# Kernel optimization log

Measured on AMD Instinct MI355X. Metric: run time of the kernel, lower is better.

## Reference

```python
import jax, jax.numpy as jnp
import numpy as np

B, T, IN, H, OUT = 1024, 512, 19, 128, 7


def setup_inputs() -> dict:
    key = jax.random.key(0)
    ks = jax.random.split(key, 12)
    k = 1.0 / np.sqrt(H)  # torch default init bound for LSTMCell/Linear
    u = lambda kk, shape: jax.random.uniform(kk, shape, jnp.float32, -k, k)
    return {
        "x": jax.random.normal(ks[0], (B, T, IN), jnp.float32),
        "W_ih1": u(ks[1], (4 * H, IN)),
        "W_hh1": u(ks[2], (4 * H, H)),
        "b_ih1": u(ks[3], (4 * H,)),
        "b_hh1": u(ks[4], (4 * H,)),
        "W_ih2": u(ks[5], (4 * H, H)),
        "W_hh2": u(ks[6], (4 * H, H)),
        "b_ih2": u(ks[7], (4 * H,)),
        "b_hh2": u(ks[8], (4 * H,)),
        "W_lin": u(ks[9], (OUT, H)),
        "b_lin": u(ks[10], (OUT,)),
    }


def _lstm_cell(x_t, h, c, W_ih, W_hh, b_ih, b_hh):
    # gates in torch order: i, f, g, o
    gates = x_t @ W_ih.T + b_ih + h @ W_hh.T + b_hh  # [B, 4H]
    i, f, g, o = jnp.split(gates, 4, axis=-1)
    c_new = jax.nn.sigmoid(f) * c + jax.nn.sigmoid(i) * jnp.tanh(g)
    h_new = jax.nn.sigmoid(o) * jnp.tanh(c_new)
    return h_new, c_new


def reference(x, W_ih1, W_hh1, b_ih1, b_hh1, W_ih2, W_hh2, b_ih2, b_hh2, W_lin, b_lin):
    n = x.shape[0]
    z = jnp.zeros((n, H), jnp.float32)

    def step(carry, x_t):
        h1, c1, h2, c2 = carry
        h1, c1 = _lstm_cell(x_t, h1, c1, W_ih1, W_hh1, b_ih1, b_hh1)
        h2, c2 = _lstm_cell(h1, h2, c2, W_ih2, W_hh2, b_ih2, b_hh2)
        y = h2 @ W_lin.T + b_lin  # [B, OUT]
        return (h1, c1, h2, c2), y

    xs = jnp.swapaxes(x, 0, 1)  # [T, B, IN]
    _, ys = jax.lax.scan(step, (z, z, z, z), xs)  # ys: [T, B, OUT]
    # torch.cat(outputs, 1) -> [B, T*OUT]
    return jnp.swapaxes(ys, 0, 1).reshape(n, -1)
```

## Files before the change

kernel.cpp:

```cpp
#include <hip/hip_runtime.h>


typedef _Float16 half8 __attribute__((ext_vector_type(8)));
typedef float f32x4 __attribute__((ext_vector_type(4)));

#define MFMA16(a, b, c) __builtin_amdgcn_mfma_f32_16x16x32_f16((a), (b), (c), 0, 0, 0)
#define BARRIER() asm volatile("s_waitcnt lgkmcnt(0)\ns_barrier" ::: "memory")
#define D_AHEAD 4
#define NSLOT 5

__device__ __forceinline__ void pin(half8& v) { asm volatile("" : "+v"(v)); }

__device__ __forceinline__ void glds16(const _Float16* g, _Float16* l) {
  __builtin_amdgcn_global_load_lds(
      (const __attribute__((address_space(1))) void*)g,
      (__attribute__((address_space(3))) void*)l, 16, 0, 0);
}

__device__ __forceinline__ float sigf(float x) {
  return __builtin_amdgcn_rcpf(1.f + __expf(-x));
}
__device__ __forceinline__ float tanhf_(float x) {
  return 1.f - 2.f * __builtin_amdgcn_rcpf(1.f + __expf(2.f * x));
}
__device__ __forceinline__ float sel4(const f32x4 a, const int lg) {
  const float v01 = (lg & 1) ? a[1] : a[0];
  const float v23 = (lg & 1) ? a[3] : a[2];
  return (lg & 2) ? v23 : v01;
}

__global__ __launch_bounds__(512) void lstm_layer1_kernel(
    const float* __restrict__ x,
    const float* __restrict__ Wih,
    const float* __restrict__ Whh,
    const float* __restrict__ bih, const float* __restrict__ bhh,
    _Float16* __restrict__ h1g)
{
  __shared__ _Float16 xls[512][12][8];
  __shared__ _Float16 hbuf[2][64][8];
  const int tid = threadIdx.x, bid = blockIdx.x;
  const int wv = tid >> 6, lane = tid & 63;
  const int lg = lane >> 4, lc = lane & 15;
  const int col = wv * 16 + lc;
  const int off0 = lg * 32 + (lc & 3) * 8;
  const int woff = ((wv * 2 + (lc >> 3)) * 4 + lg) * 8 + (lc & 7);

  half8 wih_f[4], whh_f[4][4];
  float bias[4];
#pragma unroll
  for (int g = 0; g < 4; ++g) {
    const int n = g * 128 + col;
    bias[g] = bih[n] + bhh[n];
    half8 f;
#pragma unroll
    for (int j = 0; j < 8; ++j) {
      const int k = lg * 8 + j;
      f[j] = (_Float16)((k < 19) ? Wih[n * 19 + k] : 0.f);
    }
    wih_f[g] = f;
#pragma unroll
    for (int kk = 0; kk < 4; ++kk) {
      const float* p = Whh + n * 128 + kk * 32 + lg * 8;
      half8 f2;
#pragma unroll
      for (int j = 0; j < 8; ++j) f2[j] = (_Float16)p[j];
      whh_f[g][kk] = f2;
    }
  }

  for (int i2 = tid; i2 < 512 * 96; i2 += 512) {
    const int t = i2 / 96, r = i2 - t * 96;
    const int cc = r >> 5, rr = (r >> 3) & 3, j = r & 7;
    const int k = cc * 8 + j;
    float v = 0.f;
    if (k < 19) v = x[((size_t)(bid * 4 + rr) * 512 + t) * 19 + k];
    xls[t][cc * 4 + rr][j] = (_Float16)v;
  }
  for (int i = tid; i < 1024; i += 512) ((_Float16*)hbuf)[i] = (_Float16)0.f;
  __syncthreads();

  float c = 0.f;
  _Float16* h1p = h1g + (size_t)(bid * 4 + lg) * 128 + col;
  const _Float16* xb = &xls[0][0][0] + off0;
  _Float16* hb0p = &hbuf[0][0][0];
  const f32x4 fz = {0.f, 0.f, 0.f, 0.f};
  const bool xv = (lg < 3);

#define L1_STEP(T, RD, WR)                                                    \
  {                                                                           \
    const _Float16* rd = (RD) + off0;                                         \
    const half8 hb0 = *(const half8*)(rd);                                    \
    const half8 hb1 = *(const half8*)(rd + 128);                              \
    const half8 hb2 = *(const half8*)(rd + 256);                              \
    const half8 hb3 = *(const half8*)(rd + 384);                              \
    half8 ax = {};                                                            \
    if (xv) ax = *(const half8*)(xb + (T) * 96);                              \
    f32x4 a0 = MFMA16(ax, wih_f[0], fz);                                      \
    f32x4 a1 = MFMA16(ax, wih_f[1], fz);                                      \
    f32x4 a2 = MFMA16(ax, wih_f[2], fz);                                      \
    f32x4 a3 = MFMA16(ax, wih_f[3], fz);                                      \
    a0 = MFMA16(hb0, whh_f[0][0], a0); a1 = MFMA16(hb0, whh_f[1][0], a1);     \
    a2 = MFMA16(hb0, whh_f[2][0], a2); a3 = MFMA16(hb0, whh_f[3][0], a3);     \
    a0 = MFMA16(hb1, whh_f[0][1], a0); a1 = MFMA16(hb1, whh_f[1][1], a1);     \
    a2 = MFMA16(hb1, whh_f[2][1], a2); a3 = MFMA16(hb1, whh_f[3][1], a3);     \
    a0 = MFMA16(hb2, whh_f[0][2], a0); a1 = MFMA16(hb2, whh_f[1][2], a1);     \
    a2 = MFMA16(hb2, whh_f[2][2], a2); a3 = MFMA16(hb2, whh_f[3][2], a3);     \
    a0 = MFMA16(hb3, whh_f[0][3], a0); a1 = MFMA16(hb3, whh_f[1][3], a1);     \
    a2 = MFMA16(hb3, whh_f[2][3], a2); a3 = MFMA16(hb3, whh_f[3][3], a3);     \
    const float gi = sel4(a0, lg) + bias[0];                                  \
    const float gf = sel4(a1, lg) + bias[1];                                  \
    const float gg = sel4(a2, lg) + bias[2];                                  \
    const float go = sel4(a3, lg) + bias[3];                                  \
    const float I = sigf(gi), F = sigf(gf), G = tanhf_(gg), O = sigf(go);     \
    c = F * c + I * G;                                                        \
    const float h = O * tanhf_(c);                                            \
    const _Float16 h16 = (_Float16)h;                                         \
    (WR)[woff] = h16;                                                         \
    h1p[(size_t)(T) * 131072] = h16;                                          \
    BARRIER();                                                                \
  }

#pragma unroll 1
  for (int t = 0; t < 512; t += 2) {
    L1_STEP(t, hb0p + 512, hb0p);
    L1_STEP(t + 1, hb0p, hb0p + 512);
  }
#undef L1_STEP
}

__global__ __launch_bounds__(1024) void lstm_layer2_pc(
    const _Float16* __restrict__ h1g,
    const float* __restrict__ Wih,
    const float* __restrict__ Whh,
    const float* __restrict__ bih, const float* __restrict__ bhh,
    const float* __restrict__ Wlin,
    const float* __restrict__ blin,
    float* __restrict__ out)
{
  __shared__ float ring2[NSLOT][128 * 20];
  __shared__ _Float16 h1s[4][512];
  __shared__ _Float16 h2b[2][512];
  __shared__ _Float16 wlls[16][136];
  const int tid = threadIdx.x, bid = blockIdx.x;
  const int wv = tid >> 6, lane = tid & 63;
  const int lg = lane >> 4, lc = lane & 15;
  const bool isCons = (wv < 8);
  const int cw = isCons ? wv : (wv - 8);
  const int col = cw * 16 + lc;
  const int off0 = lg * 32 + (lc & 3) * 8;
  const int woff = ((col >> 3) * 4 + lg) * 8 + (col & 7);
  const int roff = col * 20 + lg * 4;

  for (int i = tid; i < 16 * 128; i += 1024)
    wlls[i >> 7][i & 127] = (_Float16)((i < 7 * 128) ? Wlin[i] : 0.f);
  for (int i = tid; i < 1024; i += 1024) ((_Float16*)h2b)[i] = (_Float16)0.f;

  const int gchunk = (lane & 48) | ((lane & 15) ^ ((lane >> 3) & 6));
  const _Float16* h1base = h1g + (size_t)bid * 512 + gchunk * 8;
  if (wv == 8) {
    glds16(h1base, &h1s[0][0]);
    glds16(h1base + 131072, &h1s[1][0]);
    glds16(h1base + 262144, &h1s[2][0]);
    asm volatile("s_waitcnt vmcnt(2)" ::: "memory");
  }

  if (isCons) {
    half8 wh_f[4][4];
#pragma unroll
    for (int g = 0; g < 4; ++g) {
      const int n = g * 128 + col;
#pragma unroll
      for (int kk = 0; kk < 4; ++kk) {
        const float* p = Whh + n * 128 + kk * 32 + lg * 8;
        half8 f;
#pragma unroll
        for (int j = 0; j < 8; ++j) f[j] = (_Float16)p[j];
        wh_f[g][kk] = f;
      }
      pin(wh_f[g][0]); pin(wh_f[g][1]); pin(wh_f[g][2]); pin(wh_f[g][3]);
    }
    const bool yv = (lc < 7);
    const float ybias = yv ? blin[lc] : 0.f;
    const f32x4 fz = {0.f, 0.f, 0.f, 0.f};
    __syncthreads();

    float c = 0.f;
    int slotR = 0;
#pragma unroll 1
    for (int it = 0; it < 512 + D_AHEAD; ++it) {
      if (it >= D_AHEAD) {
        const int t = it - D_AHEAD;
        const int pb = t & 1;
        const _Float16* rd = &h2b[pb ^ 1][0] + off0;
        const half8 q0 = *(const half8*)(rd);
        const half8 q1 = *(const half8*)(rd + 128);
        const half8 q2 = *(const half8*)(rd + 256);
        const half8 q3 = *(const half8*)(rd + 384);
        const f32x4 rv = *(const f32x4*)(&ring2[slotR][0] + roff);
        f32x4 b0, b1, b2, b3;
        __builtin_amdgcn_s_setprio(1);
        b0 = MFMA16(q0, wh_f[0][0], fz); b1 = MFMA16(q0, wh_f[1][0], fz);
        b2 = MFMA16(q0, wh_f[2][0], fz); b3 = MFMA16(q0, wh_f[3][0], fz);
        b0 = MFMA16(q1, wh_f[0][1], b0); b1 = MFMA16(q1, wh_f[1][1], b1);
        b2 = MFMA16(q1, wh_f[2][1], b2); b3 = MFMA16(q1, wh_f[3][1], b3);
        b0 = MFMA16(q2, wh_f[0][2], b0); b1 = MFMA16(q2, wh_f[1][2], b1);
        b2 = MFMA16(q2, wh_f[2][2], b2); b3 = MFMA16(q2, wh_f[3][2], b3);
        b0 = MFMA16(q3, wh_f[0][3], b0); b1 = MFMA16(q3, wh_f[1][3], b1);
        b2 = MFMA16(q3, wh_f[2][3], b2); b3 = MFMA16(q3, wh_f[3][3], b3);
        __builtin_amdgcn_s_setprio(0);
        if (wv == 0 && t > 0) {
          const _Float16* wlp = &wlls[lc][0] + lg * 8;
          f32x4 ya = {ybias, ybias, ybias, ybias};
          {
            const half8 w0 = *(const half8*)(wlp);
            const half8 w1 = *(const half8*)(wlp + 32);
            ya = MFMA16(q0, w0, ya);
            ya = MFMA16(q1, w1, ya);
          }
          {
            const half8 w2 = *(const half8*)(wlp + 64);
            const half8 w3 = *(const half8*)(wlp + 96);
            ya = MFMA16(q2, w2, ya);
            ya = MFMA16(q3, w3, ya);
          }
          if (lg == 0 && yv) {
#pragma unroll
            for (int j = 0; j < 4; ++j)
              out[(size_t)(bid * 4 + j) * 3584 + (size_t)(t - 1) * 7 + lc] = ya[j];
          }
        }
        const float gi = sel4(b0, lg) + rv[0];
        const float gf = sel4(b1, lg) + rv[1];
        const float gg = sel4(b2, lg) + rv[2];
        const float go = sel4(b3, lg) + rv[3];
        const float I = sigf(gi), F = sigf(gf), G = tanhf_(gg), O = sigf(go);
        c = F * c + I * G;
        h2b[pb][woff] = (_Float16)(O * tanhf_(c));
        if (++slotR == NSLOT) slotR = 0;
      }
      BARRIER();
    }
    if (wv == 0) {
      const _Float16* rd = &h2b[1][0] + off0;
      const half8 q0 = *(const half8*)(rd);
      const half8 q1 = *(const half8*)(rd + 128);
      const half8 q2 = *(const half8*)(rd + 256);
      const half8 q3 = *(const half8*)(rd + 384);
      const _Float16* wlp = &wlls[lc][0] + lg * 8;
      const half8 w0 = *(const half8*)(wlp);
      const half8 w1 = *(const half8*)(wlp + 32);
      const half8 w2 = *(const half8*)(wlp + 64);
      const half8 w3 = *(const half8*)(wlp + 96);
      f32x4 ya = {ybias, ybias, ybias, ybias};
      ya = MFMA16(q0, w0, ya);
      ya = MFMA16(q1, w1, ya);
      ya = MFMA16(q2, w2, ya);
      ya = MFMA16(q3, w3, ya);
      if (lg == 0 && yv) {
#pragma unroll
        for (int j = 0; j < 4; ++j)
          out[(size_t)(bid * 4 + j) * 3584 + (size_t)511 * 7 + lc] = ya[j];
      }
    }
  } else {
    half8 wi_f[4][4];
    float bias_s[4];
#pragma unroll
    for (int g = 0; g < 4; ++g) {
      const int n = g * 128 + col;
      bias_s[g] = bih[n] + bhh[n];
#pragma unroll
      for (int kk = 0; kk < 4; ++kk) {
        const float* p = Wih + n * 128 + kk * 32 + lg * 8;
        half8 f;
#pragma unroll
        for (int j = 0; j < 8; ++j) f[j] = (_Float16)p[j];
        wi_f[g][kk] = f;
      }
      pin(wi_f[g][0]); pin(wi_f[g][1]); pin(wi_f[g][2]); pin(wi_f[g][3]);
    }
    const f32x4 bV0 = {bias_s[0], bias_s[0], bias_s[0], bias_s[0]};
    const f32x4 bV1 = {bias_s[1], bias_s[1], bias_s[1], bias_s[1]};
    const f32x4 bV2 = {bias_s[2], bias_s[2], bias_s[2], bias_s[2]};
    const f32x4 bV3 = {bias_s[3], bias_s[3], bias_s[3], bias_s[3]};
    const int hrow = lc & 3;
    int hofs[4];
#pragma unroll
    for (int kk = 0; kk < 4; ++kk)
      hofs[kk] = hrow * 128 + (((kk * 4 + lg) ^ (hrow << 1)) << 3);
    __syncthreads();

    int slotW = 0;
#pragma unroll 1
    for (int it = 0; it < 512 + D_AHEAD; ++it) {
      if (it < 512) {
        if (wv == 8 && it + 3 < 512)
          glds16(h1base + (size_t)(it + 3) * 131072, &h1s[(it + 3) & 3][0]);
        const _Float16* hp = &h1s[it & 3][0];
        const half8 p0 = *(const half8*)(hp + hofs[0]);
        const half8 p1 = *(const half8*)(hp + hofs[1]);
        const half8 p2 = *(const half8*)(hp + hofs[2]);
        const half8 p3 = *(const half8*)(hp + hofs[3]);
        f32x4 a0 = MFMA16(p0, wi_f[0][0], bV0);
        f32x4 a1 = MFMA16(p0, wi_f[1][0], bV1);
        f32x4 a2 = MFMA16(p0, wi_f[2][0], bV2);
        f32x4 a3 = MFMA16(p0, wi_f[3][0], bV3);
        a0 = MFMA16(p1, wi_f[0][1], a0); a1 = MFMA16(p1, wi_f[1][1], a1);
        a2 = MFMA16(p1, wi_f[2][1], a2); a3 = MFMA16(p1, wi_f[3][1], a3);
        a0 = MFMA16(p2, wi_f[0][2], a0); a1 = MFMA16(p2, wi_f[1][2], a1);
        a2 = MFMA16(p2, wi_f[2][2], a2); a3 = MFMA16(p2, wi_f[3][2], a3);
        a0 = MFMA16(p3, wi_f[0][3], a0); a1 = MFMA16(p3, wi_f[1][3], a1);
        a2 = MFMA16(p3, wi_f[2][3], a2); a3 = MFMA16(p3, wi_f[3][3], a3);
        {
          f32x4 v;
          v[0] = sel4(a0, lg);
          v[1] = sel4(a1, lg);
          v[2] = sel4(a2, lg);
          v[3] = sel4(a3, lg);
          *(f32x4*)(&ring2[slotW][0] + roff) = v;
        }
        if (wv == 8) asm volatile("s_waitcnt vmcnt(2)" ::: "memory");
        if (++slotW == NSLOT) slotW = 0;
      }
      BARRIER();
    }
  }
}

extern "C" void kernel_launch(void* const* d_in, const int* in_sizes, int n_in,
                              void* d_out, int out_size, void* d_ws, size_t ws_size,
                              hipStream_t stream) {
  (void)in_sizes; (void)n_in; (void)out_size; (void)ws_size;
  const float* x     = (const float*)d_in[0];
  const float* W_ih1 = (const float*)d_in[1];
  const float* W_hh1 = (const float*)d_in[2];
  const float* b_ih1 = (const float*)d_in[3];
  const float* b_hh1 = (const float*)d_in[4];
  const float* W_ih2 = (const float*)d_in[5];
  const float* W_hh2 = (const float*)d_in[6];
  const float* b_ih2 = (const float*)d_in[7];
  const float* b_hh2 = (const float*)d_in[8];
  const float* W_lin = (const float*)d_in[9];
  const float* b_lin = (const float*)d_in[10];
  float* out = (float*)d_out;
  _Float16* h1g = (_Float16*)d_ws;

  lstm_layer1_kernel<<<256, 512, 0, stream>>>(x, W_ih1, W_hh1, b_ih1, b_hh1, h1g);
  lstm_layer2_pc<<<256, 1024, 0, stream>>>(h1g, W_ih2, W_hh2, b_ih2, b_hh2,
                                           W_lin, b_lin, out);
}
```

Before: 691.0 us.

## Split layer-1 LSTM across twice the blocks with direct x prefetch and folded bias

```diff
diff --git a/kernel.cpp b/kernel.cpp
--- a/kernel.cpp
+++ b/kernel.cpp
@@ -17,6 +17,12 @@
       (__attribute__((address_space(3))) void*)l, 16, 0, 0);
 }
 
+__device__ __forceinline__ f32x4 ldg4u(const float* p) {
+  f32x4 v;
+  __builtin_memcpy(&v, p, 16);
+  return v;
+}
+
 __device__ __forceinline__ float sigf(float x) {
   return __builtin_amdgcn_rcpf(1.f + __expf(-x));
 }
@@ -29,33 +35,34 @@
   return (lg & 2) ? v23 : v01;
 }
 
-__global__ __launch_bounds__(512) void lstm_layer1_kernel(
+__global__ __launch_bounds__(512) void lstm_layer1_v2(
     const float* __restrict__ x,
     const float* __restrict__ Wih,
     const float* __restrict__ Whh,
     const float* __restrict__ bih, const float* __restrict__ bhh,
     _Float16* __restrict__ h1g)
 {
-  __shared__ _Float16 xls[512][12][8];
-  __shared__ _Float16 hbuf[2][64][8];
+  __shared__ _Float16 hbuf[2][256];
   const int tid = threadIdx.x, bid = blockIdx.x;
   const int wv = tid >> 6, lane = tid & 63;
   const int lg = lane >> 4, lc = lane & 15;
   const int col = wv * 16 + lc;
-  const int off0 = lg * 32 + (lc & 3) * 8;
-  const int woff = ((wv * 2 + (lc >> 3)) * 4 + lg) * 8 + (lc & 7);
+  const int r2 = lc & 1;
+  const int off0 = (lg * 2 + r2) * 8;
+  const int woff = ((col >> 3) * 2 + (lg & 1)) * 8 + (col & 7);
 
   half8 wih_f[4], whh_f[4][4];
-  float bias[4];
 #pragma unroll
   for (int g = 0; g < 4; ++g) {
     const int n = g * 128 + col;
-    bias[g] = bih[n] + bhh[n];
     half8 f;
 #pragma unroll
     for (int j = 0; j < 8; ++j) {
       const int k = lg * 8 + j;
-      f[j] = (_Float16)((k < 19) ? Wih[n * 19 + k] : 0.f);
+      float v = 0.f;
+      if (k < 19) v = Wih[n * 19 + k];
+      else if (k == 19) v = bih[n] + bhh[n];
+      f[j] = (_Float16)v;
     }
     wih_f[g] = f;
 #pragma unroll
@@ -68,64 +75,80 @@
     }
   }
 
-  for (int i2 = tid; i2 < 512 * 96; i2 += 512) {
-    const int t = i2 / 96, r = i2 - t * 96;
-    const int cc = r >> 5, rr = (r >> 3) & 3, j = r & 7;
-    const int k = cc * 8 + j;
-    float v = 0.f;
-    if (k < 19) v = x[((size_t)(bid * 4 + rr) * 512 + t) * 19 + k];
-    xls[t][cc * 4 + rr][j] = (_Float16)v;
-  }
-  for (int i = tid; i < 1024; i += 512) ((_Float16*)hbuf)[i] = (_Float16)0.f;
+  for (int i = tid; i < 512; i += 512) {
+    hbuf[0][i & 255] = (_Float16)0.f;
+    hbuf[1][i & 255] = (_Float16)0.f;
+  }
   __syncthreads();
 
+  const float* xr = x + (size_t)(bid * 2 + r2) * 512 * 19;
   float c = 0.f;
-  _Float16* h1p = h1g + (size_t)(bid * 4 + lg) * 128 + col;
-  const _Float16* xb = &xls[0][0][0] + off0;
-  _Float16* hb0p = &hbuf[0][0][0];
+  _Float16* h1p = h1g + (size_t)(bid * 2 + (lg & 1)) * 128 + col;
+  const bool wr2 = (lg < 2);
   const f32x4 fz = {0.f, 0.f, 0.f, 0.f};
-  const bool xv = (lg < 3);
-
-#define L1_STEP(T, RD, WR)                                                    \
+
+#define LOADX(DST, T)                                                         \
   {                                                                           \
-    const _Float16* rd = (RD) + off0;                                         \
-    const half8 hb0 = *(const half8*)(rd);                                    \
-    const half8 hb1 = *(const half8*)(rd + 128);                              \
-    const half8 hb2 = *(const half8*)(rd + 256);                              \
-    const half8 hb3 = *(const half8*)(rd + 384);                              \
-    half8 ax = {};                                                            \
-    if (xv) ax = *(const half8*)(xb + (T) * 96);                              \
-    f32x4 a0 = MFMA16(ax, wih_f[0], fz);                                      \
-    f32x4 a1 = MFMA16(ax, wih_f[1], fz);                                      \
-    f32x4 a2 = MFMA16(ax, wih_f[2], fz);                                      \
-    f32x4 a3 = MFMA16(ax, wih_f[3], fz);                                      \
-    a0 = MFMA16(hb0, whh_f[0][0], a0); a1 = MFMA16(hb0, whh_f[1][0], a1);     \
-    a2 = MFMA16(hb0, whh_f[2][0], a2); a3 = MFMA16(hb0, whh_f[3][0], a3);     \
-    a0 = MFMA16(hb1, whh_f[0][1], a0); a1 = MFMA16(hb1, whh_f[1][1], a1);     \
-    a2 = MFMA16(hb1, whh_f[2][1], a2); a3 = MFMA16(hb1, whh_f[3][1], a3);     \
-    a0 = MFMA16(hb2, whh_f[0][2], a0); a1 = MFMA16(hb2, whh_f[1][2], a1);     \
-    a2 = MFMA16(hb2, whh_f[2][2], a2); a3 = MFMA16(hb2, whh_f[3][2], a3);     \
-    a0 = MFMA16(hb3, whh_f[0][3], a0); a1 = MFMA16(hb3, whh_f[1][3], a1);     \
-    a2 = MFMA16(hb3, whh_f[2][3], a2); a3 = MFMA16(hb3, whh_f[3][3], a3);     \
-    const float gi = sel4(a0, lg) + bias[0];                                  \
-    const float gf = sel4(a1, lg) + bias[1];                                  \
-    const float gg = sel4(a2, lg) + bias[2];                                  \
-    const float go = sel4(a3, lg) + bias[3];                                  \
-    const float I = sigf(gi), F = sigf(gf), G = tanhf_(gg), O = sigf(go);     \
-    c = F * c + I * G;                                                        \
-    const float h = O * tanhf_(c);                                            \
-    const _Float16 h16 = (_Float16)h;                                         \
-    (WR)[woff] = h16;                                                         \
-    h1p[(size_t)(T) * 131072] = h16;                                          \
-    BARRIER();                                                                \
-  }
+    half8 f = {};                                                             \
+    const float* xp_ = xr + (size_t)(T) * 19;                                 \
+    if (lg < 2) {                                                             \
+      const f32x4 u0 = ldg4u(xp_ + lg * 8);                                   \
+      const f32x4 u1 = ldg4u(xp_ + lg * 8 + 4);                               \
+      f[0] = (_Float16)u0[0]; f[1] = (_Float16)u0[1];                         \
+      f[2] = (_Float16)u0[2]; f[3] = (_Float16)u0[3];                         \
+      f[4] = (_Float16)u1[0]; f[5] = (_Float16)u1[1];                         \
+      f[6] = (_Float16)u1[2]; f[7] = (_Float16)u1[3];                         \
+    } else if (lg == 2) {                                                     \
+      const f32x4 u = ldg4u(xp_ + 15);   \
+      f[0] = (_Float16)u[1]; f[1] = (_Float16)u[2];                           \
+      f[2] = (_Float16)u[3]; f[3] = (_Float16)1.f;                            \
+    }                                                                         \
+    DST = f;                                                                  \
+  }
+
+  half8 xcur, xnext;
+  LOADX(xcur, 0);
 
 #pragma unroll 1
-  for (int t = 0; t < 512; t += 2) {
-    L1_STEP(t, hb0p + 512, hb0p);
-    L1_STEP(t + 1, hb0p, hb0p + 512);
-  }
-#undef L1_STEP
+  for (int t = 0; t < 512; ++t) {
+    const _Float16* rd = &hbuf[(t & 1) ^ 1][0] + off0;
+    const half8 hb0 = *(const half8*)(rd);
+    const half8 hb1 = *(const half8*)(rd + 64);
+    const half8 hb2 = *(const half8*)(rd + 128);
+    const half8 hb3 = *(const half8*)(rd + 192);
+    if (t + 1 < 512) {
+      LOADX(xnext, t + 1);
+    } else {
+      xnext = xcur;
+    }
+    f32x4 a0 = MFMA16(xcur, wih_f[0], fz);
+    f32x4 a1 = MFMA16(xcur, wih_f[1], fz);
+    f32x4 a2 = MFMA16(xcur, wih_f[2], fz);
+    f32x4 a3 = MFMA16(xcur, wih_f[3], fz);
+    a0 = MFMA16(hb0, whh_f[0][0], a0); a1 = MFMA16(hb0, whh_f[1][0], a1);
+    a2 = MFMA16(hb0, whh_f[2][0], a2); a3 = MFMA16(hb0, whh_f[3][0], a3);
+    a0 = MFMA16(hb1, whh_f[0][1], a0); a1 = MFMA16(hb1, whh_f[1][1], a1);
+    a2 = MFMA16(hb1, whh_f[2][1], a2); a3 = MFMA16(hb1, whh_f[3][1], a3);
+    a0 = MFMA16(hb2, whh_f[0][2], a0); a1 = MFMA16(hb2, whh_f[1][2], a1);
+    a2 = MFMA16(hb2, whh_f[2][2], a2); a3 = MFMA16(hb2, whh_f[3][2], a3);
+    a0 = MFMA16(hb3, whh_f[0][3], a0); a1 = MFMA16(hb3, whh_f[1][3], a1);
+    a2 = MFMA16(hb3, whh_f[2][3], a2); a3 = MFMA16(hb3, whh_f[3][3], a3);
+    const float gi = (lg & 1) ? a0[1] : a0[0];
+    const float gf = (lg & 1) ? a1[1] : a1[0];
+    const float gg = (lg & 1) ? a2[1] : a2[0];
+    const float go = (lg & 1) ? a3[1] : a3[0];
+    const float I = sigf(gi), F = sigf(gf), G = tanhf_(gg), O = sigf(go);
+    c = F * c + I * G;
+    const float h = O * tanhf_(c);
+    if (wr2) {
+      const _Float16 h16 = (_Float16)h;
+      hbuf[t & 1][woff] = h16;
+      h1p[(size_t)t * 131072] = h16;
+    }
+    xcur = xnext;
+    BARRIER();
+  }
+#undef LOADX
 }
 
 __global__ __launch_bounds__(1024) void lstm_layer2_pc(
@@ -345,7 +368,7 @@
   float* out = (float*)d_out;
   _Float16* h1g = (_Float16*)d_ws;
 
-  lstm_layer1_kernel<<<256, 512, 0, stream>>>(x, W_ih1, W_hh1, b_ih1, b_hh1, h1g);
+  lstm_layer1_v2<<<512, 512, 0, stream>>>(x, W_ih1, W_hh1, b_ih1, b_hh1, h1g);
   lstm_layer2_pc<<<256, 1024, 0, stream>>>(h1g, W_ih2, W_hh2, b_ih2, b_hh2,
                                            W_lin, b_lin, out);
 }
```

After: 1.259 ms. 1.82x slower.
